# Kernel optimization log

Hardware: AMD Instinct MI355X
Metric: run time of the kernel (lower is better)

The kernel has to match this reference:

```python
import jax, jax.numpy as jnp
import numpy as np

NEG_INF = -1e9


def setup_inputs() -> dict:
    key = jax.random.key(0)
    ks = jax.random.split(key, 7)
    N, Q, C = 16, 4096, 77
    D, Dc, H, S = 512, 768, 8, 64
    scale = 0.02
    return {
        "query": jax.random.normal(ks[0], (N, Q, D), jnp.float32),
        "context": jax.random.normal(ks[1], (N, C, Dc), jnp.float32),
        "Wq": jax.random.normal(ks[2], (D, H, S), jnp.float32) * scale,
        "Wk": jax.random.normal(ks[3], (Dc, H, S), jnp.float32) * scale,
        "Wv": jax.random.normal(ks[4], (Dc, H, S), jnp.float32) * scale,
        "Wo": jax.random.normal(ks[5], (H, S, D), jnp.float32) * scale,
        "bo": jnp.zeros((D,), jnp.float32),
    }


def reference(query, context, Wq, Wk, Wv, Wo, bo):
    # Projections: split hidden dim into heads.
    q = jnp.einsum('NQD,DHS->NQHS', query, Wq)      # [N,Q,H,S]
    k = jnp.einsum('NCD,DHS->NCHS', context, Wk)    # [N,C,H,S]
    v = jnp.einsum('NCD,DHS->NCHS', context, Wv)    # [N,C,H,S]
    size_per_head = q.shape[-1]
    # Attention scores [N,H,Q,C], scaled by 1/sqrt(S).
    scores = jnp.einsum('NQHS,NCHS->NHQC', q, k) * (size_per_head ** -0.5)
    weights = jax.nn.softmax(scores, axis=3)
    out = jnp.einsum('NHQC,NCHS->NQHS', weights, v)  # [N,Q,H,S]
    # Merge heads back to model dim with output bias.
    return jnp.einsum('NQHS,HSD->NQD', out, Wo) + bo
```

## Files before the change

kernel.cpp:

```cpp
#include <hip/hip_runtime.h>

typedef unsigned short u16;
typedef unsigned int u32;
typedef __bf16 bf16_t;
typedef bf16_t bf16x8 __attribute__((ext_vector_type(8)));
typedef float floatx4 __attribute__((ext_vector_type(4)));

__device__ __forceinline__ float bf2f(u16 h) {
    union { unsigned u; float f; } v;
    v.u = ((unsigned)h) << 16;
    return v.f;
}

__device__ __forceinline__ u16 f2bf(float f) {
    union { float f; unsigned u; } v;
    v.f = f;
    unsigned r = v.u + 0x7fffu + ((v.u >> 16) & 1u);
    return (u16)(r >> 16);
}

typedef __attribute__((address_space(1))) const u32 gu32;
typedef __attribute__((address_space(3))) u32 lu32;
__device__ __forceinline__ void gload16(const void* g, void* l) {
    __builtin_amdgcn_global_load_lds((gu32*)g, (lu32*)l, 16, 0, 0);
}

__global__ void transpose_one(const float* __restrict__ W, u16* __restrict__ Wt,
                              int K, int N, float scale) {
    int idx = blockIdx.x * 256 + threadIdx.x;
    if (idx >= K * N) return;
    int nrow = idx / K;
    int k = idx - nrow * K;
    Wt[idx] = f2bf(W[k * N + nrow] * scale);
}

__global__ void transpose_kv(const float* __restrict__ Wk, const float* __restrict__ Wv,
                             u16* __restrict__ Wt) {
    int idx = blockIdx.x * 256 + threadIdx.x;
    if (idx >= 1024 * 768) return;
    int nrow = idx / 768;
    int k = idx - nrow * 768;
    Wt[idx] = f2bf((nrow < 512) ? Wk[k * 512 + nrow] : Wv[k * 512 + (nrow - 512)]);
}

__global__ void transpose_v(const u16* __restrict__ kv, u16* __restrict__ vt) {
    int idx = blockIdx.x * 256 + threadIdx.x;
    if (idx >= 16 * 8 * 64 * 96) return;
    int c  = idx % 96;
    int t1 = idx / 96;
    int s  = t1 & 63;
    int t2 = t1 >> 6;
    int h  = t2 & 7;
    int n  = t2 >> 3;
    u16 val = 0;
    if (c < 77) val = kv[((long)(n * 77 + c)) * 1024 + 512 + h * 64 + s];
    vt[idx] = val;
}

#define TM 128
#define TN 256
#define TK 32

template <bool A_F32, bool OUT_F32>
__global__ __launch_bounds__(512, 4) void gemm_bt(
    const void* __restrict__ A_, const u16* __restrict__ Bt,
    void* __restrict__ C_, const float* __restrict__ bias,
    int M, int K, int N, int ntl2)
{
    constexpr int AB = A_F32 ? TM * TK * 4 : TM * TK * 2;
    constexpr int BB = TN * TK * 2;
    __shared__ __align__(16) char smem[2 * (AB + BB)];

    const int tid  = threadIdx.x;
    const int lane = tid & 63;
    const int wave = tid >> 6;
    const int quad = lane >> 4;
    const int l16  = lane & 15;
    const int wm   = (wave & 1) * 64;
    const int wn   = (wave >> 1) * 64;

    const int nwg = gridDim.x;
    const int wg  = blockIdx.x;
    const int t   = (wg & 7) * (nwg >> 3) + (wg >> 3);
    const long bm = (long)(t >> ntl2) * TM;
    const long bn = (long)(t & ((1 << ntl2) - 1)) * TN;

    const float* Af = (const float*)A_;
    const u16*   Ab = (const u16*)A_;
    const long   Mm1 = (long)M - 1;

    floatx4 acc[4][4] = {};

    auto stage = [&](int b, int k0) {
        char* Abase = smem + b * (AB + BB);
        u16*  Bb    = (u16*)(Abase + AB);
        #pragma unroll
        for (int p = 0; p < 2; ++p) {
            int ch  = p * 512 + tid;
            int row = ch >> 2;
            int pc  = (ch & 3) ^ ((row >> 1) & 3);
            gload16(Bt + (bn + row) * K + k0 + pc * 8,
                    Bb + (p * 512 + wave * 64) * 8);
        }
        if (A_F32) {
            #pragma unroll
            for (int p = 0; p < 2; ++p) {
                int ch  = p * 512 + tid;
                int row = ch >> 3;
                int pcs = (ch & 7) ^ (row & 7);
                long gr = bm + row; if (gr > Mm1) gr = Mm1;
                gload16(Af + gr * K + k0 + pcs * 4,
                        (float*)Abase + (p * 512 + wave * 64) * 4);
            }
        } else {
            int row = tid >> 2;
            int pc  = (tid & 3) ^ ((row >> 1) & 3);
            long gr = bm + row; if (gr > Mm1) gr = Mm1;
            gload16(Ab + gr * K + k0 + pc * 8,
                    (u16*)Abase + (wave * 64) * 8);
        }
    };

    const int nk = K / TK;
    stage(0, 0);

    for (int tt = 0; tt < nk; ++tt) {
        const int cb = tt & 1;
        if (tt + 1 < nk) {
            stage(cb ^ 1, (tt + 1) * TK);
            if (A_F32) asm volatile("s_waitcnt vmcnt(4)" ::: "memory");
            else       asm volatile("s_waitcnt vmcnt(3)" ::: "memory");
        } else {
            asm volatile("s_waitcnt vmcnt(0)" ::: "memory");
        }
        __builtin_amdgcn_s_barrier();
        __builtin_amdgcn_sched_barrier(0);

        const char* Abase = smem + cb * (AB + BB);
        const u16*  Bb    = (const u16*)(Abase + AB);

        bf16x8 af[4], bfr[4];
        #pragma unroll
        for (int i = 0; i < 4; ++i) {
            int row = wm + i * 16 + l16;
            if (A_F32) {
                const char* arow = Abase + (size_t)row * 128;
                int x = row & 7;
                float4 f0 = *(const float4*)(arow + (((quad * 2)     ^ x) * 16));
                float4 f1 = *(const float4*)(arow + (((quad * 2 + 1) ^ x) * 16));
                union { bf16_t h[8]; bf16x8 v; } pk;
                pk.h[0] = (bf16_t)f0.x; pk.h[1] = (bf16_t)f0.y;
                pk.h[2] = (bf16_t)f0.z; pk.h[3] = (bf16_t)f0.w;
                pk.h[4] = (bf16_t)f1.x; pk.h[5] = (bf16_t)f1.y;
                pk.h[6] = (bf16_t)f1.z; pk.h[7] = (bf16_t)f1.w;
                af[i] = pk.v;
            } else {
                int pcs = quad ^ ((row >> 1) & 3);
                af[i] = *(const bf16x8*)((const u16*)Abase + row * 32 + pcs * 8);
            }
        }
        #pragma unroll
        for (int j = 0; j < 4; ++j) {
            int row = wn + j * 16 + l16;
            int pcs = quad ^ ((row >> 1) & 3);
            bfr[j] = *(const bf16x8*)(Bb + row * 32 + pcs * 8);
        }
        #pragma unroll
        for (int i = 0; i < 4; ++i)
            #pragma unroll
            for (int j = 0; j < 4; ++j)
                acc[i][j] = __builtin_amdgcn_mfma_f32_16x16x32_bf16(
                    af[i], bfr[j], acc[i][j], 0, 0, 0);

        __builtin_amdgcn_s_barrier();
    }

    #pragma unroll
    for (int i = 0; i < 4; ++i) {
        #pragma unroll
        for (int r = 0; r < 4; ++r) {
            long row = bm + wm + i * 16 + quad * 4 + r;
            if (row >= M) continue;
            #pragma unroll
            for (int j = 0; j < 4; ++j) {
                long col = bn + wn + j * 16 + l16;
                float val = acc[i][j][r];
                if (bias) val += bias[col];
                if (OUT_F32) ((float*)C_)[row * N + col] = val;
                else         ((u16*)C_)[row * N + col] = f2bf(val);
            }
        }
    }
}

__global__ __launch_bounds__(512, 4) void attn_kernel(
    const u16* __restrict__ qb,
    const u16* __restrict__ kvb,
    const u16* __restrict__ vt,
    u16* __restrict__ ob)
{
    const int QL = 4096, HS = 512;
    const int q0 = blockIdx.x * 256;
    const int h  = blockIdx.y;
    const int n  = blockIdx.z;

    __shared__ u16 ks [80 * 72];
    __shared__ u16 vts[64 * 104];
    __shared__ u16 pS [8][32 * 104];

    const int tid  = threadIdx.x;
    const int lane = tid & 63;
    const int wave = tid >> 6;
    const int quad = lane >> 4;
    const int l16  = lane & 15;

    const long qrow = (long)n * QL + q0 + wave * 32;
    bf16x8 aq[2][2];
    #pragma unroll
    for (int t = 0; t < 2; ++t)
        #pragma unroll
        for (int kk = 0; kk < 2; ++kk)
            aq[t][kk] = *(const bf16x8*)(
                qb + (qrow + t * 16 + l16) * HS + h * 64 + kk * 32 + quad * 8);

    const u16* kbase = kvb + (long)n * 77 * 1024 + h * 64;
    for (int v = tid; v < 640; v += 512) {
        int c = v >> 3, g = (v & 7) * 8;
        uint4 val = make_uint4(0, 0, 0, 0);
        if (c < 77) val = *(const uint4*)(kbase + (long)c * 1024 + g);
        *(uint4*)(&ks[c * 72 + g]) = val;
    }
    const u16* vtbase = vt + (long)((n * 8 + h) * 64) * 96;
    for (int v = tid; v < 768; v += 512) {
        int r = v / 12, c8 = v - r * 12;
        *(uint4*)(&vts[r * 104 + c8 * 8]) = *(const uint4*)(vtbase + v * 8);
    }
    __syncthreads();

    floatx4 accS[2][5] = {};
    #pragma unroll
    for (int kk = 0; kk < 2; ++kk) {
        bf16x8 bk[5];
        #pragma unroll
        for (int j = 0; j < 5; ++j)
            bk[j] = *(const bf16x8*)(&ks[(j * 16 + l16) * 72 + kk * 32 + quad * 8]);
        #pragma unroll
        for (int t = 0; t < 2; ++t)
            #pragma unroll
            for (int j = 0; j < 5; ++j)
                accS[t][j] = __builtin_amdgcn_mfma_f32_16x16x32_bf16(
                    aq[t][kk], bk[j], accS[t][j], 0, 0, 0);
    }

    const bool v4ok = (l16 < 13);
    u16* pw = pS[wave];
    #pragma unroll
    for (int t = 0; t < 2; ++t) {
        #pragma unroll
        for (int r = 0; r < 4; ++r) {
            float v0 = accS[t][0][r];
            float v1 = accS[t][1][r];
            float v2 = accS[t][2][r];
            float v3 = accS[t][3][r];
            float v4 = v4ok ? accS[t][4][r] : -1e30f;
            float mx = fmaxf(fmaxf(fmaxf(v0, v1), fmaxf(v2, v3)), v4);
            mx = fmaxf(mx, __shfl_xor(mx, 1));
            mx = fmaxf(mx, __shfl_xor(mx, 2));
            mx = fmaxf(mx, __shfl_xor(mx, 4));
            mx = fmaxf(mx, __shfl_xor(mx, 8));
            float e0 = __expf(v0 - mx), e1 = __expf(v1 - mx);
            float e2 = __expf(v2 - mx), e3 = __expf(v3 - mx);
            float e4 = __expf(v4 - mx);
            float sum = e0 + e1 + e2 + e3 + e4;
            sum += __shfl_xor(sum, 1);
            sum += __shfl_xor(sum, 2);
            sum += __shfl_xor(sum, 4);
            sum += __shfl_xor(sum, 8);
            float inv = 1.f / sum;
            int row = t * 16 + quad * 4 + r;
            pw[row * 104 +  0 + l16] = f2bf(e0 * inv);
            pw[row * 104 + 16 + l16] = f2bf(e1 * inv);
            pw[row * 104 + 32 + l16] = f2bf(e2 * inv);
            pw[row * 104 + 48 + l16] = f2bf(e3 * inv);
            pw[row * 104 + 64 + l16] = f2bf(e4 * inv);
            pw[row * 104 + 80 + l16] = 0;
        }
    }

    floatx4 accO[2][4] = {};
    #pragma unroll
    for (int kk = 0; kk < 3; ++kk) {
        bf16x8 aw[2], bv[4];
        #pragma unroll
        for (int t = 0; t < 2; ++t)
            aw[t] = *(const bf16x8*)(&pw[(t * 16 + l16) * 104 + kk * 32 + quad * 8]);
        #pragma unroll
        for (int j = 0; j < 4; ++j)
            bv[j] = *(const bf16x8*)(&vts[(j * 16 + l16) * 104 + kk * 32 + quad * 8]);
        #pragma unroll
        for (int t = 0; t < 2; ++t)
            #pragma unroll
            for (int j = 0; j < 4; ++j)
                accO[t][j] = __builtin_amdgcn_mfma_f32_16x16x32_bf16(
                    aw[t], bv[j], accO[t][j], 0, 0, 0);
    }

    u16* obase = ob + qrow * HS + h * 64;
    #pragma unroll
    for (int t = 0; t < 2; ++t)
        #pragma unroll
        for (int j = 0; j < 4; ++j)
            #pragma unroll
            for (int r = 0; r < 4; ++r) {
                int row = t * 16 + quad * 4 + r;
                obase[(long)row * HS + j * 16 + l16] = f2bf(accO[t][j][r]);
            }
}

extern "C" void kernel_launch(void* const* d_in, const int* in_sizes, int n_in,
                              void* d_out, int out_size, void* d_ws, size_t ws_size,
                              hipStream_t stream) {
    const float* query   = (const float*)d_in[0];
    const float* context = (const float*)d_in[1];
    const float* Wq      = (const float*)d_in[2];
    const float* Wk      = (const float*)d_in[3];
    const float* Wv      = (const float*)d_in[4];
    const float* Wo      = (const float*)d_in[5];
    const float* bo      = (const float*)d_in[6];
    float* out = (float*)d_out;

    u16* q_ws  = (u16*)d_ws;
    u16* kv_ws = q_ws + 33554432;
    u16* WqT   = kv_ws + 1261568;
    u16* WkvT  = WqT + 262144;
    u16* WoT   = WkvT + 786432;
    u16* vt_ws = WkvT;

    transpose_one<<<(512 * 512 + 255) / 256, 256, 0, stream>>>(Wq, WqT, 512, 512, 0.125f);
    transpose_kv<<<(1024 * 768 + 255) / 256, 256, 0, stream>>>(Wk, Wv, WkvT);
    transpose_one<<<(512 * 512 + 255) / 256, 256, 0, stream>>>(Wo, WoT, 512, 512, 1.0f);

    gemm_bt<true, false><<<dim3(1024), 512, 0, stream>>>(
        (const void*)query, WqT, (void*)q_ws, nullptr, 65536, 512, 512, 1);
    gemm_bt<true, false><<<dim3(40), 512, 0, stream>>>(
        (const void*)context, WkvT, (void*)kv_ws, nullptr, 1232, 768, 1024, 2);
    transpose_v<<<(16 * 8 * 64 * 96 + 255) / 256, 256, 0, stream>>>(kv_ws, vt_ws);
    attn_kernel<<<dim3(16, 8, 16), 512, 0, stream>>>(q_ws, kv_ws, vt_ws, q_ws);
    gemm_bt<false, true><<<dim3(1024), 512, 0, stream>>>(
        q_ws, WoT, (void*)out, bo, 65536, 512, 512, 1);
}
```

Before: 405.4 us.

## Use LDS-free direct-load GEMM, set MFMA priority, stage attention output stores

Adds a GEMM variant that loads A and B fragments straight from global memory into registers, skipping shared-memory staging, and uses it for the Q projection and the output projection. The attention kernel raises wave priority around its MFMA blocks. It also writes its output tile to LDS first and then copies it out with 16-byte vector stores instead of scattered 2-byte stores. The direct GEMM gives up LDS reuse and double buffering, so its global loads are redundant across waves and only partly coalesced, and it relies on the cache to absorb them.

Result: slower. 598.1 us (+47.5%).

```diff
diff --git a/kernel.cpp b/kernel.cpp
--- a/kernel.cpp
+++ b/kernel.cpp
@@ -55,6 +55,86 @@
     u16 val = 0;
     if (c < 77) val = kv[((long)(n * 77 + c)) * 1024 + 512 + h * 64 + s];
     vt[idx] = val;
+}
+
+template <bool A_F32, bool OUT_F32>
+__global__ __launch_bounds__(512, 4) void gemm_direct(
+    const void* __restrict__ A_, const u16* __restrict__ Bt,
+    void* __restrict__ C_, const float* __restrict__ bias,
+    int M, int K, int N, int ntl2)
+{
+    const int tid  = threadIdx.x;
+    const int lane = tid & 63;
+    const int wave = tid >> 6;
+    const int quad = lane >> 4;
+    const int l16  = lane & 15;
+    const int wm   = (wave & 1) * 64;
+    const int wn   = (wave >> 1) * 64;
+
+    const int nwg = gridDim.x;
+    const int wg  = blockIdx.x;
+    const int t   = (wg & 7) * (nwg >> 3) + (wg >> 3);
+    const long bm = (long)(t >> ntl2) * 128;
+    const long bn = (long)(t & ((1 << ntl2) - 1)) * 256;
+
+    const float* Af = (const float*)A_;
+    const u16*   Ab = (const u16*)A_;
+
+    long arow[4], brow[4];
+    #pragma unroll
+    for (int i = 0; i < 4; ++i)
+        arow[i] = (bm + wm + i * 16 + l16) * (long)K + quad * 8;
+    #pragma unroll
+    for (int j = 0; j < 4; ++j)
+        brow[j] = (bn + wn + j * 16 + l16) * (long)K + quad * 8;
+
+    floatx4 acc[4][4] = {};
+
+    #pragma unroll 2
+    for (int k0 = 0; k0 < K; k0 += 32) {
+        bf16x8 af[4], bfr[4];
+        #pragma unroll
+        for (int i = 0; i < 4; ++i) {
+            if (A_F32) {
+                const float* ap = Af + arow[i] + k0;
+                float4 f0 = *(const float4*)ap;
+                float4 f1 = *(const float4*)(ap + 4);
+                union { bf16_t h[8]; bf16x8 v; } pk;
+                pk.h[0] = (bf16_t)f0.x; pk.h[1] = (bf16_t)f0.y;
+                pk.h[2] = (bf16_t)f0.z; pk.h[3] = (bf16_t)f0.w;
+                pk.h[4] = (bf16_t)f1.x; pk.h[5] = (bf16_t)f1.y;
+                pk.h[6] = (bf16_t)f1.z; pk.h[7] = (bf16_t)f1.w;
+                af[i] = pk.v;
+            } else {
+                af[i] = *(const bf16x8*)(Ab + arow[i] + k0);
+            }
+        }
+        #pragma unroll
+        for (int j = 0; j < 4; ++j)
+            bfr[j] = *(const bf16x8*)(Bt + brow[j] + k0);
+        #pragma unroll
+        for (int i = 0; i < 4; ++i)
+            #pragma unroll
+            for (int j = 0; j < 4; ++j)
+                acc[i][j] = __builtin_amdgcn_mfma_f32_16x16x32_bf16(
+                    af[i], bfr[j], acc[i][j], 0, 0, 0);
+    }
+
+    #pragma unroll
+    for (int i = 0; i < 4; ++i) {
+        #pragma unroll
+        for (int r = 0; r < 4; ++r) {
+            long row = bm + wm + i * 16 + quad * 4 + r;
+            #pragma unroll
+            for (int j = 0; j < 4; ++j) {
+                long col = bn + wn + j * 16 + l16;
+                float val = acc[i][j][r];
+                if (bias) val += bias[col];
+                if (OUT_F32) ((float*)C_)[row * N + col] = val;
+                else         ((u16*)C_)[row * N + col] = f2bf(val);
+            }
+        }
+    }
 }
 
 #define TM 128
@@ -244,12 +324,14 @@
         #pragma unroll
         for (int j = 0; j < 5; ++j)
             bk[j] = *(const bf16x8*)(&ks[(j * 16 + l16) * 72 + kk * 32 + quad * 8]);
+        __builtin_amdgcn_s_setprio(1);
         #pragma unroll
         for (int t = 0; t < 2; ++t)
             #pragma unroll
             for (int j = 0; j < 5; ++j)
                 accS[t][j] = __builtin_amdgcn_mfma_f32_16x16x32_bf16(
                     aq[t][kk], bk[j], accS[t][j], 0, 0, 0);
+        __builtin_amdgcn_s_setprio(0);
     }
 
     const bool v4ok = (l16 < 13);
@@ -297,15 +379,16 @@
         #pragma unroll
         for (int j = 0; j < 4; ++j)
             bv[j] = *(const bf16x8*)(&vts[(j * 16 + l16) * 104 + kk * 32 + quad * 8]);
+        __builtin_amdgcn_s_setprio(1);
         #pragma unroll
         for (int t = 0; t < 2; ++t)
             #pragma unroll
             for (int j = 0; j < 4; ++j)
                 accO[t][j] = __builtin_amdgcn_mfma_f32_16x16x32_bf16(
                     aw[t], bv[j], accO[t][j], 0, 0, 0);
-    }
-
-    u16* obase = ob + qrow * HS + h * 64;
+        __builtin_amdgcn_s_setprio(0);
+    }
+
     #pragma unroll
     for (int t = 0; t < 2; ++t)
         #pragma unroll
@@ -313,8 +396,18 @@
             #pragma unroll
             for (int r = 0; r < 4; ++r) {
                 int row = t * 16 + quad * 4 + r;
-                obase[(long)row * HS + j * 16 + l16] = f2bf(accO[t][j][r]);
-            }
+                pw[row * 72 + j * 16 + l16] = f2bf(accO[t][j][r]);
+            }
+
+    u16* obase = ob + qrow * HS + h * 64;
+    #pragma unroll
+    for (int k = 0; k < 4; ++k) {
+        int v   = k * 64 + lane;
+        int row = v >> 3;
+        int c8  = v & 7;
+        *(uint4*)(obase + (long)row * HS + c8 * 8) =
+            *(const uint4*)(&pw[row * 72 + c8 * 8]);
+    }
 }
 
 extern "C" void kernel_launch(void* const* d_in, const int* in_sizes, int n_in,
@@ -340,12 +433,12 @@
     transpose_kv<<<(1024 * 768 + 255) / 256, 256, 0, stream>>>(Wk, Wv, WkvT);
     transpose_one<<<(512 * 512 + 255) / 256, 256, 0, stream>>>(Wo, WoT, 512, 512, 1.0f);
 
-    gemm_bt<true, false><<<dim3(1024), 512, 0, stream>>>(
+    gemm_direct<true, false><<<dim3(1024), 512, 0, stream>>>(
         (const void*)query, WqT, (void*)q_ws, nullptr, 65536, 512, 512, 1);
     gemm_bt<true, false><<<dim3(40), 512, 0, stream>>>(
         (const void*)context, WkvT, (void*)kv_ws, nullptr, 1232, 768, 1024, 2);
     transpose_v<<<(16 * 8 * 64 * 96 + 255) / 256, 256, 0, stream>>>(kv_ws, vt_ws);
     attn_kernel<<<dim3(16, 8, 16), 512, 0, stream>>>(q_ws, kv_ws, vt_ws, q_ws);
-    gemm_bt<false, true><<<dim3(1024), 512, 0, stream>>>(
+    gemm_direct<false, true><<<dim3(1024), 512, 0, stream>>>(
         q_ws, WoT, (void*)out, bo, 65536, 512, 512, 1);
 }
```
